# Performance work log

Hardware: AMD Instinct MI355X
Metric: run time of the kernel (lower is better)

The kernel has to match this reference:

```python
import jax, jax.numpy as jnp
import numpy as np

D_ORIG, D_HEAD, N_HEAD = 64, 32, 8
D_EMB = D_HEAD * N_HEAD


def setup_inputs() -> dict:
    key = jax.random.key(0)
    ks = jax.random.split(key, 9)
    b, l = 1, 512
    x = jax.random.normal(ks[0], (b, l, D_ORIG), dtype=jnp.float32)
    e = jax.random.normal(ks[1], (b, l, l, D_ORIG), dtype=jnp.float32)
    s = 1.0 / np.sqrt(D_ORIG)
    Wq = jax.random.uniform(ks[2], (D_ORIG, D_EMB), jnp.float32, -s, s)
    Wk = jax.random.uniform(ks[3], (D_ORIG, D_EMB), jnp.float32, -s, s)
    Wv = jax.random.uniform(ks[4], (D_ORIG, D_EMB), jnp.float32, -s, s)
    We = jax.random.uniform(ks[5], (D_ORIG, D_EMB), jnp.float32, -s, s)
    so = 1.0 / np.sqrt(D_EMB)
    Wo = jax.random.uniform(ks[6], (D_EMB, D_ORIG), jnp.float32, -so, so)
    bo = jax.random.uniform(ks[7], (D_ORIG,), jnp.float32, -so, so)
    return {"x": x, "e": e, "Wq": Wq, "Wk": Wk, "Wv": Wv, "We": We, "Wo": Wo, "bo": bo}


def reference(x, e, Wq, Wk, Wv, We, Wo, bo):
    b, l, _ = x.shape
    # projections
    q = (x @ Wq).reshape(b, l, N_HEAD, D_HEAD).transpose(0, 2, 1, 3)  # b n l d
    k = (x @ Wk).reshape(b, l, N_HEAD, D_HEAD).transpose(0, 2, 1, 3)
    v = (x @ Wv).reshape(b, l, N_HEAD, D_HEAD).transpose(0, 2, 1, 3)
    ee = (e @ We).reshape(b, l, l, N_HEAD, D_HEAD).transpose(0, 3, 1, 2, 4)  # b n i j d
    # edge-biased keys/values: broadcast add over query index i
    kb = k[:, :, None, :, :] + ee  # b n i j d
    logit = jnp.einsum('bnid,bnijd->bnij', q, kb) * (D_HEAD ** -0.5)
    attn = jax.nn.softmax(logit, axis=-1)
    vb = v[:, :, None, :, :] + ee  # b n i j d
    out = jnp.einsum('bnij,bnijd->bnid', attn, vb)  # b n i d
    out = out.transpose(0, 2, 1, 3).reshape(b, l, D_EMB)
    return out @ Wo + bo
```

## Files before the change

### kernel.cpp

```cpp
#include <hip/hip_runtime.h>

#define SCALE 0.17677669529663687f
#define PSTR 516

#define FMA64(E, X, qc)                                                         \
  {                                                                             \
    const float* _q = (qc);                                                     \
    _Pragma("unroll")                                                           \
    for (int h = 0; h < 8; ++h)                                                 \
      acc[h] += (E).x * _q[h]      + (E).y * _q[16 + h]                         \
              + (E).z * _q[32 + h] + (E).w * _q[48 + h]                         \
              + (X).x * _q[8 + h]  + (X).y * _q[24 + h]                         \
              + (X).z * _q[40 + h] + (X).w * _q[56 + h];                        \
  }

__global__ __launch_bounds__(512, 4) void fused_kernel(
    const float* __restrict__ e, const float* __restrict__ x,
    const float* __restrict__ Wq, const float* __restrict__ Wk,
    const float* __restrict__ We, const float* __restrict__ Wv,
    const float* __restrict__ Wo, const float* __restrict__ bo,
    float* __restrict__ out) {
  const int t = threadIdx.x, i = blockIdx.x;
  __shared__ float s_x[64];
  __shared__ __align__(16) float s_q[256];
  __shared__ __align__(16) float s_qc[1024];
  __shared__ __align__(16) float s_p[8 * PSTR];
  __shared__ __align__(16) float s_part[8 * 1024];
  __shared__ float s_ae[512], s_px[512];
  __shared__ float s_emb[256];
  __shared__ float s_op[8 * 64];

  if (t < 64) s_x[t] = x[i * 64 + t];
  __syncthreads();
  if (t < 256) {
    float a = 0;
#pragma unroll 8
    for (int c = 0; c < 64; ++c) a += s_x[c] * Wq[c * 256 + t];
    s_q[t] = a * SCALE;
  }
  __syncthreads();
  {
    const int c = t >> 3, h = t & 7;
    const float4* wer = (const float4*)(We + c * 256 + h * 32);
    const float4* wkr = (const float4*)(Wk + c * 256 + h * 32);
    const float4* qr = (const float4*)(s_q + h * 32);
    float se = 0, sk = 0;
#pragma unroll
    for (int u = 0; u < 8; ++u) {
      float4 w1 = wer[u], w2 = wkr[u], qv = qr[u];
      se += qv.x * w1.x + qv.y * w1.y + qv.z * w1.z + qv.w * w1.w;
      sk += qv.x * w2.x + qv.y * w2.y + qv.z * w2.z + qv.w * w2.w;
    }
    s_qc[c * 16 + h] = se;
    s_qc[c * 16 + 8 + h] = sk;
  }
  __syncthreads();

  {
    const int j = t;
    const float4* erow = (const float4*)(e + (size_t)(i * 512 + j) * 64);
    const float4* xrow = (const float4*)(x + j * 64);
    float4 Eb[8], Xb[8];
#pragma unroll
    for (int u = 0; u < 8; ++u) Eb[u] = erow[u];
#pragma unroll
    for (int u = 0; u < 8; ++u) Xb[u] = xrow[u];
    float acc[8];
#pragma unroll
    for (int h = 0; h < 8; ++h) acc[h] = 0.f;
#pragma unroll
    for (int u = 0; u < 8; ++u) {
      FMA64(Eb[u], Xb[u], s_qc + u * 64);
      Eb[u] = erow[8 + u];
      Xb[u] = xrow[8 + u];
    }
#pragma unroll
    for (int u = 0; u < 8; ++u) FMA64(Eb[u], Xb[u], s_qc + (8 + u) * 64);
#pragma unroll
    for (int h = 0; h < 8; ++h) s_p[h * PSTR + j] = acc[h];
  }
  __syncthreads();

  {
    const int n = t >> 6, l64 = t & 63;
    float m = -1e30f;
#pragma unroll
    for (int u = 0; u < 8; ++u) m = fmaxf(m, s_p[n * PSTR + l64 + u * 64]);
#pragma unroll
    for (int off = 32; off; off >>= 1) m = fmaxf(m, __shfl_xor(m, off, 64));
    float pv[8];
    float sum = 0;
#pragma unroll
    for (int u = 0; u < 8; ++u) {
      pv[u] = __expf(s_p[n * PSTR + l64 + u * 64] - m);
      sum += pv[u];
    }
#pragma unroll
    for (int off = 32; off; off >>= 1) sum += __shfl_xor(sum, off, 64);
    const float inv = 1.0f / sum;
#pragma unroll
    for (int u = 0; u < 8; ++u) s_p[n * PSTR + l64 + u * 64] = pv[u] * inv;
  }
  __syncthreads();

  {
    const int lane = t & 63, w = t >> 6;
    float ae[8], px[8];
#pragma unroll
    for (int h = 0; h < 8; ++h) { ae[h] = 0.f; px[h] = 0.f; }
    const float* ep = e + (size_t)i * 32768 + (size_t)w * 4096 + lane;
    const float* xp = x + w * 4096 + lane;
    for (int jb = 0; jb < 64; jb += 8) {
      float ev[8], xv[8];
#pragma unroll
      for (int u = 0; u < 8; ++u) ev[u] = ep[(jb + u) * 64];
#pragma unroll
      for (int u = 0; u < 8; ++u) xv[u] = xp[(jb + u) * 64];
      const int j0 = w * 64 + jb;
#pragma unroll
      for (int h = 0; h < 8; ++h) {
        float4 pa = *(const float4*)&s_p[h * PSTR + j0];
        float4 pb = *(const float4*)&s_p[h * PSTR + j0 + 4];
        ae[h] += pa.x * ev[0] + pa.y * ev[1] + pa.z * ev[2] + pa.w * ev[3]
               + pb.x * ev[4] + pb.y * ev[5] + pb.z * ev[6] + pb.w * ev[7];
        px[h] += pa.x * xv[0] + pa.y * xv[1] + pa.z * xv[2] + pa.w * xv[3]
               + pb.x * xv[4] + pb.y * xv[5] + pb.z * xv[6] + pb.w * xv[7];
      }
    }
#pragma unroll
    for (int h = 0; h < 8; ++h) {
      s_part[w * 1024 + h * 64 + lane] = ae[h];
      s_part[w * 1024 + 512 + h * 64 + lane] = px[h];
    }
  }
  __syncthreads();

  {
    float va = 0, vp = 0;
#pragma unroll
    for (int w = 0; w < 8; ++w) {
      va += s_part[w * 1024 + t];
      vp += s_part[w * 1024 + 512 + t];
    }
    s_ae[t] = va; s_px[t] = vp;
  }
  __syncthreads();

  {
    const int nd = t & 255, ch = t >> 8, hn = nd >> 5;
    float emb = 0;
    const int cb = ch * 32;
#pragma unroll 8
    for (int c = cb; c < cb + 32; ++c)
      emb += s_ae[hn * 64 + c] * We[c * 256 + nd] + s_px[hn * 64 + c] * Wv[c * 256 + nd];
    s_part[ch * 256 + nd] = emb;
  }
  __syncthreads();
  if (t < 256) s_emb[t] = s_part[t] + s_part[256 + t];
  __syncthreads();
  {
    const int o = t & 63, mc = t >> 6;
    float oo = 0;
#pragma unroll 8
    for (int m2 = mc * 32; m2 < mc * 32 + 32; ++m2) oo += s_emb[m2] * Wo[m2 * 64 + o];
    s_op[mc * 64 + o] = oo;
  }
  __syncthreads();
  if (t < 64) {
    float r = bo[t];
#pragma unroll
    for (int w = 0; w < 8; ++w) r += s_op[w * 64 + t];
    out[i * 64 + t] = r;
  }
}

extern "C" void kernel_launch(void* const* d_in, const int* in_sizes, int n_in,
                              void* d_out, int out_size, void* d_ws, size_t ws_size,
                              hipStream_t stream) {
  const float* x  = (const float*)d_in[0];
  const float* e  = (const float*)d_in[1];
  const float* Wq = (const float*)d_in[2];
  const float* Wk = (const float*)d_in[3];
  const float* Wv = (const float*)d_in[4];
  const float* We = (const float*)d_in[5];
  const float* Wo = (const float*)d_in[6];
  const float* bo = (const float*)d_in[7];
  float* out = (float*)d_out;

  hipLaunchKernelGGL(fused_kernel, dim3(512), dim3(512), 0, stream,
                     e, x, Wq, Wk, We, Wv, Wo, bo, out);
}
```

Measured before the change: 143.7 us.

## Stagger e-row chunk order per wave and double-buffer e loads across softmax

Drops the shared staging of x for the q projection and reads x directly from global memory. The logit pass now keeps a 4-deep rotating register buffer and starts each wave at a different 64-byte column chunk, which lowers register pressure and spreads memory-channel access. The aggregation pass double-buffers its strided e/x loads and issues the first batch before the softmax barrier, so global latency overlaps the softmax. The extra live registers across the softmax could lower occupancy under launch_bounds(512,4).

```diff
diff --git a/kernel.cpp b/kernel.cpp
--- a/kernel.cpp
+++ b/kernel.cpp
@@ -21,7 +21,6 @@
     const float* __restrict__ Wo, const float* __restrict__ bo,
     float* __restrict__ out) {
   const int t = threadIdx.x, i = blockIdx.x;
-  __shared__ float s_x[64];
   __shared__ __align__(16) float s_q[256];
   __shared__ __align__(16) float s_qc[1024];
   __shared__ __align__(16) float s_p[8 * PSTR];
@@ -30,12 +29,11 @@
   __shared__ float s_emb[256];
   __shared__ float s_op[8 * 64];
 
-  if (t < 64) s_x[t] = x[i * 64 + t];
-  __syncthreads();
   if (t < 256) {
+    const float* xr = x + i * 64;
     float a = 0;
 #pragma unroll 8
-    for (int c = 0; c < 64; ++c) a += s_x[c] * Wq[c * 256 + t];
+    for (int c = 0; c < 64; ++c) a += xr[c] * Wq[c * 256 + t];
     s_q[t] = a * SCALE;
   }
   __syncthreads();
@@ -56,33 +54,48 @@
   }
   __syncthreads();
 
+  const int wv = t >> 6;
+  const int lane = t & 63;
+
   {
     const int j = t;
     const float4* erow = (const float4*)(e + (size_t)(i * 512 + j) * 64);
     const float4* xrow = (const float4*)(x + j * 64);
-    float4 Eb[8], Xb[8];
-#pragma unroll
-    for (int u = 0; u < 8; ++u) Eb[u] = erow[u];
-#pragma unroll
-    for (int u = 0; u < 8; ++u) Xb[u] = xrow[u];
+    const int coff = (wv * 2) & 15;
+    float4 Eb[4], Xb[4];
+#pragma unroll
+    for (int u = 0; u < 4; ++u) {
+      const int c = (coff + u) & 15;
+      Eb[u] = erow[c];
+      Xb[u] = xrow[c];
+    }
     float acc[8];
 #pragma unroll
     for (int h = 0; h < 8; ++h) acc[h] = 0.f;
 #pragma unroll
-    for (int u = 0; u < 8; ++u) {
-      FMA64(Eb[u], Xb[u], s_qc + u * 64);
-      Eb[u] = erow[8 + u];
-      Xb[u] = xrow[8 + u];
-    }
-#pragma unroll
-    for (int u = 0; u < 8; ++u) FMA64(Eb[u], Xb[u], s_qc + (8 + u) * 64);
+    for (int u = 0; u < 16; ++u) {
+      const int c = (coff + u) & 15;
+      const int slot = u & 3;
+      FMA64(Eb[slot], Xb[slot], s_qc + c * 64);
+      if (u < 12) {
+        const int cn = (coff + u + 4) & 15;
+        Eb[slot] = erow[cn];
+        Xb[slot] = xrow[cn];
+      }
+    }
 #pragma unroll
     for (int h = 0; h < 8; ++h) s_p[h * PSTR + j] = acc[h];
   }
-  __syncthreads();
-
-  {
-    const int n = t >> 6, l64 = t & 63;
+
+  const float* ep = e + (size_t)i * 32768 + (size_t)wv * 4096 + lane;
+  const float* xp = x + wv * 4096 + lane;
+  float evb[2][8], xvb[2][8];
+#pragma unroll
+  for (int u = 0; u < 8; ++u) { evb[0][u] = ep[u * 64]; xvb[0][u] = xp[u * 64]; }
+  __syncthreads();
+
+  {
+    const int n = wv, l64 = lane;
     float m = -1e30f;
 #pragma unroll
     for (int u = 0; u < 8; ++u) m = fmaxf(m, s_p[n * PSTR + l64 + u * 64]);
@@ -104,33 +117,38 @@
   __syncthreads();
 
   {
-    const int lane = t & 63, w = t >> 6;
     float ae[8], px[8];
 #pragma unroll
     for (int h = 0; h < 8; ++h) { ae[h] = 0.f; px[h] = 0.f; }
-    const float* ep = e + (size_t)i * 32768 + (size_t)w * 4096 + lane;
-    const float* xp = x + w * 4096 + lane;
-    for (int jb = 0; jb < 64; jb += 8) {
-      float ev[8], xv[8];
-#pragma unroll
-      for (int u = 0; u < 8; ++u) ev[u] = ep[(jb + u) * 64];
-#pragma unroll
-      for (int u = 0; u < 8; ++u) xv[u] = xp[(jb + u) * 64];
-      const int j0 = w * 64 + jb;
+#pragma unroll
+    for (int jb = 0; jb < 8; ++jb) {
+      const int cur = jb & 1, nxt = cur ^ 1;
+      if (jb < 7) {
+#pragma unroll
+        for (int u = 0; u < 8; ++u) {
+          evb[nxt][u] = ep[((jb + 1) * 8 + u) * 64];
+          xvb[nxt][u] = xp[((jb + 1) * 8 + u) * 64];
+        }
+      }
+      const int j0 = wv * 64 + jb * 8;
 #pragma unroll
       for (int h = 0; h < 8; ++h) {
         float4 pa = *(const float4*)&s_p[h * PSTR + j0];
         float4 pb = *(const float4*)&s_p[h * PSTR + j0 + 4];
-        ae[h] += pa.x * ev[0] + pa.y * ev[1] + pa.z * ev[2] + pa.w * ev[3]
-               + pb.x * ev[4] + pb.y * ev[5] + pb.z * ev[6] + pb.w * ev[7];
-        px[h] += pa.x * xv[0] + pa.y * xv[1] + pa.z * xv[2] + pa.w * xv[3]
-               + pb.x * xv[4] + pb.y * xv[5] + pb.z * xv[6] + pb.w * xv[7];
+        ae[h] += pa.x * evb[cur][0] + pa.y * evb[cur][1]
+               + pa.z * evb[cur][2] + pa.w * evb[cur][3]
+               + pb.x * evb[cur][4] + pb.y * evb[cur][5]
+               + pb.z * evb[cur][6] + pb.w * evb[cur][7];
+        px[h] += pa.x * xvb[cur][0] + pa.y * xvb[cur][1]
+               + pa.z * xvb[cur][2] + pa.w * xvb[cur][3]
+               + pb.x * xvb[cur][4] + pb.y * xvb[cur][5]
+               + pb.z * xvb[cur][6] + pb.w * xvb[cur][7];
       }
     }
 #pragma unroll
     for (int h = 0; h < 8; ++h) {
-      s_part[w * 1024 + h * 64 + lane] = ae[h];
-      s_part[w * 1024 + 512 + h * 64 + lane] = px[h];
+      s_part[wv * 1024 + h * 64 + lane] = ae[h];
+      s_part[wv * 1024 + 512 + h * 64 + lane] = px[h];
     }
   }
   __syncthreads();
```

Measured after the change: 151.7 us. 5.6% more time.
